# Kernel optimization log

Hardware: AMD Instinct MI355X
Metric: run time of the kernel (lower is better)

Reference implementation:

```python
import jax, jax.numpy as jnp
import numpy as np

B, S, IN_DIM, D_MODEL, H = 8, 1024, 512, 1024, 16
DEPTH = D_MODEL // H
LN_EPS = 1e-5


def setup_inputs() -> dict:
    key = jax.random.key(0)
    ks = jax.random.split(key, 10)
    def xavier(k, shape):
        fan_in, fan_out = shape[0], shape[1]
        lim = float(np.sqrt(6.0 / (fan_in + fan_out)))
        return jax.random.uniform(k, shape, jnp.float32, -lim, lim)
    return {
        "x": jax.random.normal(ks[0], (B, S, IN_DIM), jnp.float32),
        "mask": jax.random.randint(ks[1], (H, S, S), 0, 2, jnp.int32),
        "wq_w": xavier(ks[2], (IN_DIM, D_MODEL)),
        "wq_b": jnp.zeros((D_MODEL,), jnp.float32),
        "wk_w": xavier(ks[3], (IN_DIM, D_MODEL)),
        "wk_b": jnp.zeros((D_MODEL,), jnp.float32),
        "wv_w": xavier(ks[4], (IN_DIM, D_MODEL)),
        "wv_b": jnp.zeros((D_MODEL,), jnp.float32),
        "dense_w": xavier(ks[5], (D_MODEL, D_MODEL)),
        "dense_b": jnp.zeros((D_MODEL,), jnp.float32),
        "res_w": xavier(ks[6], (IN_DIM, D_MODEL)),  # residual_linear (no bias)
        "ln_g": 1.0 + 0.02 * jax.random.normal(ks[7], (D_MODEL,), jnp.float32),
        "ln_b": 0.02 * jax.random.normal(ks[8], (D_MODEL,), jnp.float32),
    }


def reference(x, mask, wq_w, wq_b, wk_w, wk_b, wv_w, wv_b,
              dense_w, dense_b, res_w, ln_g, ln_b):
    bs = x.shape[0]
    residual = x @ res_w  # [B,S,D_MODEL]
    # project and split heads -> [B,H,S,depth]
    def split(t):
        return t.reshape(bs, -1, H, DEPTH).transpose(0, 2, 1, 3)
    q = split(x @ wq_w + wq_b)
    k = split(x @ wk_w + wk_b)
    v = split(x @ wv_w + wv_b)
    scale = 1.0 / jnp.sqrt(jnp.asarray(DEPTH, x.dtype))
    attn = jnp.einsum("bhqd,bhkd->bhqk", q, k) * scale
    attn = jnp.where(mask[None] == 0, jnp.asarray(-1e9, attn.dtype), attn)
    attn = jax.nn.softmax(attn, axis=-1)  # dropout is identity in eval
    out = jnp.einsum("bhqk,bhkd->bhqd", attn, v)
    out = out.transpose(0, 2, 1, 3).reshape(bs, -1, D_MODEL)
    out = out @ dense_w + dense_b
    # residual + LayerNorm
    y = residual + out
    mu = jnp.mean(y, axis=-1, keepdims=True)
    var = jnp.mean(jnp.square(y - mu), axis=-1, keepdims=True)
    y = (y - mu) * jax.lax.rsqrt(var + LN_EPS)
    return y * ln_g + ln_b
```

## Files before the change

### kernel.cpp

```cpp
#include <hip/hip_runtime.h>
#include <stdint.h>

#define B_ 8
#define S_ 1024
#define IN_DIM 512
#define DM 1024
#define H_ 16
#define DEP 64

typedef __bf16 bf16;
typedef __attribute__((ext_vector_type(8))) __bf16 bf16x8;
typedef __attribute__((ext_vector_type(4))) __bf16 bf16x4;
typedef __attribute__((ext_vector_type(4))) short short4v;
typedef __attribute__((ext_vector_type(4))) float f32x4;

#if defined(__has_builtin)
#if __has_builtin(__builtin_amdgcn_mfma_f32_16x16x16_bf16)
#define HAVE_NEW16 1
#endif
#endif
static __device__ __forceinline__ f32x4 mfma16(bf16x4 a, bf16x4 b, f32x4 c) {
#ifdef HAVE_NEW16
    return __builtin_amdgcn_mfma_f32_16x16x16_bf16(a, b, c, 0, 0, 0);
#else
    union { bf16x4 h; short4v s; } ua, ub;
    ua.h = a; ub.h = b;
    return __builtin_amdgcn_mfma_f32_16x16x16bf16_1k(ua.s, ub.s, c, 0, 0, 0);
#endif
}

static __device__ __forceinline__ void gld_lds16(const void* g, void* l) {
    __builtin_amdgcn_global_load_lds(
        (const __attribute__((address_space(1))) uint32_t*)g,
        (__attribute__((address_space(3))) uint32_t*)l, 16, 0, 0);
}

__global__ void detect_kernel(const uint16_t* __restrict__ xraw, int* __restrict__ flag) {
    const int t = threadIdx.x;
    int sane = 0;
    #pragma unroll
    for (int j = 0; j < 8; j++) {
        const uint16_t u = xraw[t * 8 + j];
        const int e = (u >> 7) & 0xff;
        sane += ((u & 0x7fff) == 0 || (e >= 100 && e <= 140)) ? 1 : 0;
    }
    #pragma unroll
    for (int m = 1; m < 64; m <<= 1) sane += __shfl_xor(sane, m);
    if (t == 0) *flag = (sane >= 450) ? 1 : 0;
}

static __device__ __forceinline__ float ldin(const void* p, size_t i, int isb) {
    return isb ? (float)((const bf16*)p)[i] : ((const float*)p)[i];
}

__global__ __launch_bounds__(256) void transpose_kernel(
    const void* __restrict__ wq, const void* __restrict__ wk, const void* __restrict__ wv,
    const void* __restrict__ res, const void* __restrict__ dense,
    bf16* __restrict__ wqT, bf16* __restrict__ wkT, bf16* __restrict__ wvT,
    bf16* __restrict__ resT, bf16* __restrict__ denseT, const int* __restrict__ flag)
{
    const int isb = *flag;
    __shared__ bf16 tile[32][33];
    const int z = blockIdx.z;
    const void* src; bf16* dst; int kb, kd;
    if (z == 0)      { src = wq;    dst = wqT;    kb = 0;   kd = 512;  }
    else if (z == 1) { src = wk;    dst = wkT;    kb = 0;   kd = 512;  }
    else if (z == 2) { src = wv;    dst = wvT;    kb = 0;   kd = 512;  }
    else if (z == 3) { src = res;   dst = resT;   kb = 0;   kd = 512;  }
    else if (z == 4) { src = dense; dst = denseT; kb = 0;   kd = 1024; }
    else             { src = dense; dst = denseT; kb = 512; kd = 1024; }
    const int n0 = blockIdx.x * 32, k0 = blockIdx.y * 32;
    const int tx = threadIdx.x, ty = threadIdx.y;
    #pragma unroll
    for (int r = 0; r < 4; r++)
        tile[ty + r*8][tx] = (bf16)ldin(src, (size_t)(kb + k0 + ty + r*8) * DM + n0 + tx, isb);
    __syncthreads();
    #pragma unroll
    for (int r = 0; r < 4; r++)
        dst[(size_t)(n0 + ty + r*8) * kd + kb + k0 + tx] = tile[tx][ty + r*8];
}

__global__ __launch_bounds__(256) void xconv_kernel(
    const void* __restrict__ x, bf16* __restrict__ xc, const int* __restrict__ flag)
{
    const int isb = *flag;
    const size_t i = ((size_t)blockIdx.x * 256 + threadIdx.x) * 4;
    #pragma unroll
    for (int j = 0; j < 4; j++) xc[i + j] = (bf16)ldin(x, i + j, isb);
}

__global__ __launch_bounds__(256) void smallconv_kernel(
    const void* b0, const void* b1, const void* b2, const void* b3,
    const void* b4, const void* b5, bf16* __restrict__ out, const int* __restrict__ flag)
{
    const int isb = *flag;
    const void* srcs[6] = {b0, b1, b2, b3, b4, b5};
    const void* s = srcs[blockIdx.x];
    for (int i = threadIdx.x; i < 1024; i += 256)
        out[blockIdx.x * 1024 + i] = (bf16)ldin(s, i, isb);
}

__global__ __launch_bounds__(256) void maskpack_kernel(
    const int* __restrict__ mask, unsigned long long* __restrict__ mb)
{
    const int w = threadIdx.x >> 6, lane = threadIdx.x & 63;
    const int gw = blockIdx.x * 4 + w;
    for (int c = gw; c < 262144; c += 4096) {
        const int v = mask[(size_t)c * 64 + lane];
        const unsigned long long bits = __ballot(v != 0);
        if (lane == 0) mb[c] = bits;
    }
}

template<int KDIM>
static __device__ __forceinline__ void gemm_core(
    const bf16* __restrict__ A, const bf16* __restrict__ BT,
    int m0, int n0, bf16* Asm, bf16* Bsm, f32x4 acc[4][4])
{
    const int tid = threadIdx.x, l = tid & 63, w = tid >> 6;
    const int wm = w >> 1, wn = w & 1, quad = l >> 4, l15 = l & 15;
    #pragma unroll
    for (int i = 0; i < 4; i++)
        #pragma unroll
        for (int j = 0; j < 4; j++) acc[i][j] = f32x4{0.f, 0.f, 0.f, 0.f};

    for (int k0 = 0; k0 < KDIM; k0 += 32) {
        __syncthreads();
        #pragma unroll
        for (int qq = 0; qq < 2; qq++) {
            const int c = qq*256 + tid;
            const int row = c >> 2, ch = c & 3;
            gld_lds16(A  + (size_t)(m0 + row)*KDIM + k0 + ch*8, Asm + (qq*256 + w*64)*8);
            gld_lds16(BT + (size_t)(n0 + row)*KDIM + k0 + ch*8, Bsm + (qq*256 + w*64)*8);
        }
        __syncthreads();
        bf16x8 af[4], bfv[4];
        #pragma unroll
        for (int i = 0; i < 4; i++)
            af[i] = *(const bf16x8*)(Asm + (wm*64 + i*16 + l15)*32 + quad*8);
        #pragma unroll
        for (int j = 0; j < 4; j++)
            bfv[j] = *(const bf16x8*)(Bsm + (wn*64 + j*16 + l15)*32 + quad*8);
        #pragma unroll
        for (int i = 0; i < 4; i++)
            #pragma unroll
            for (int j = 0; j < 4; j++)
                acc[i][j] = __builtin_amdgcn_mfma_f32_16x16x32_bf16(af[i], bfv[j], acc[i][j], 0, 0, 0);
    }
}

#define EPI_P 132
__global__ __launch_bounds__(256) void proj_kernel(
    const bf16* __restrict__ x,
    const bf16* __restrict__ wqT, const bf16* __restrict__ wkT,
    const bf16* __restrict__ wvT, const bf16* __restrict__ resT,
    const bf16* __restrict__ small,
    bf16* __restrict__ Q, bf16* __restrict__ K, bf16* __restrict__ VtG, bf16* __restrict__ R)
{
    __shared__ alignas(16) char smem[17408];
    bf16* Asm = (bf16*)smem;
    bf16* Bsm = (bf16*)(smem + 8192);
    bf16* epi = (bf16*)smem;

    const int m0 = blockIdx.x * 128;
    const int ng = blockIdx.y * 128;
    const int sel = ng >> 10, n0 = ng & 1023;
    const bf16* BT; const bf16* bias = nullptr;
    if (sel == 0)      { BT = wqT; bias = small;        }
    else if (sel == 1) { BT = wkT; bias = small + 1024; }
    else if (sel == 2) { BT = wvT; bias = small + 2048; }
    else               { BT = resT; }

    f32x4 acc[4][4];
    gemm_core<IN_DIM>(x, BT, m0, n0, Asm, Bsm, acc);

    const int tid = threadIdx.x, l = tid & 63, w = tid >> 6;
    const int wm = w >> 1, wn = w & 1, quad = l >> 4, l15 = l & 15;

    if (sel == 2) {
        const int bb = m0 >> 10, srow0 = m0 & 1023;
        #pragma unroll
        for (int hf = 0; hf < 2; hf++) {
            __syncthreads();
            if (wn == hf) {
                #pragma unroll
                for (int j = 0; j < 4; j++) {
                    const int cl = j*16 + l15;
                    const float bv = (float)bias[n0 + hf*64 + cl];
                    #pragma unroll
                    for (int i = 0; i < 4; i++) {
                        const int rho = wm*64 + i*16 + quad*4;
                        #pragma unroll
                        for (int r = 0; r < 4; r++)
                            epi[cl*EPI_P + rho + r] = (bf16)(acc[i][j][r] + bv);
                    }
                }
            }
            __syncthreads();
            const int hh = (n0 >> 6) + hf;
            const int sc = tid & 15;
            #pragma unroll
            for (int pass = 0; pass < 4; pass++) {
                const int dl = (tid >> 4) + pass*16;
                bf16x8 v;
                #pragma unroll
                for (int k = 0; k < 8; k++) v[k] = epi[dl*EPI_P + sc*8 + k];
                *(bf16x8*)(VtG + ((size_t)(bb*16 + hh)*64 + dl)*S_ + srow0 + sc*8) = v;
            }
        }
        return;
    }

    #pragma unroll
    for (int j = 0; j < 4; j++) {
        const int col = n0 + wn*64 + j*16 + l15;
        const float bv = (sel < 3) ? (float)bias[col] : 0.f;
        #pragma unroll
        for (int i = 0; i < 4; i++) {
            const int rb = m0 + wm*64 + i*16 + quad*4;
            #pragma unroll
            for (int r = 0; r < 4; r++) {
                const float v = acc[i][j][r] + bv;
                if (sel == 0)      Q[(size_t)(rb + r)*DM + col] = (bf16)(v * 0.18033688f);
                else if (sel == 1) K[(size_t)(rb + r)*DM + col] = (bf16)v;
                else               R[(size_t)(rb + r)*DM + col] = (bf16)v;
            }
        }
    }
}

__global__ __launch_bounds__(256, 4) void attn_kernel(
    const bf16* __restrict__ Q, const bf16* __restrict__ K, const bf16* __restrict__ VtG,
    const unsigned long long* __restrict__ mb, bf16* __restrict__ AO)
{
    __shared__ alignas(16) bf16 Ksm[2*64*64];
    __shared__ alignas(16) bf16 Vsm[2*64*64];

    const int tid = threadIdx.x, l = tid & 63, w = tid >> 6;
    const int quad = l >> 4, l15 = l & 15;

    const int fid = blockIdx.y * 8 + blockIdx.x;
    const int xcd = fid & 7, idx = fid >> 3;
    const int bh  = xcd * 16 + (idx >> 3);
    const int qt  = idx & 7;
    const int b = bh >> 4, h = bh & 15;
    const int wrow = qt*128 + w*32;
    const size_t rowbase = (size_t)b * S_;

    bf16x8 qa[2][2];
    #pragma unroll
    for (int g = 0; g < 2; g++) {
        const bf16* qp = Q + (rowbase + wrow + g*16 + l15)*DM + h*DEP + quad*8;
        qa[g][0] = *(const bf16x8*)qp;
        qa[g][1] = *(const bf16x8*)(qp + 32);
    }
    const bf16* kgbase = K + rowbase*DM + h*DEP;
    const bf16* vgbase = VtG + (size_t)(b*16 + h)*64*S_;
    const unsigned long long* mbase[2];
    #pragma unroll
    for (int g = 0; g < 2; g++)
        mbase[g] = mb + ((size_t)h*S_ + wrow + g*16 + l15) * 16;

    uint32_t bmr[4];
    #pragma unroll
    for (int r = 0; r < 4; r++) bmr[r] = 1u << (quad*4 + r);

    bf16x4 onesv;
    #pragma unroll
    for (int r = 0; r < 4; r++) onesv[r] = (bf16)1.0f;

    f32x4 oT[2][4];
    f32x4 lacc[2];
    #pragma unroll
    for (int g = 0; g < 2; g++) {
        lacc[g] = f32x4{0.f,0.f,0.f,0.f};
        #pragma unroll
        for (int dt = 0; dt < 4; dt++) oT[g][dt] = f32x4{0.f,0.f,0.f,0.f};
    }

    const int srow8 = l >> 3;
    const int gch   = (l & 7) ^ srow8;

    #pragma unroll
    for (int q = 0; q < 2; q++) {
        const int row = q*32 + w*8 + srow8;
        gld_lds16(kgbase + (size_t)row*DM + gch*8, Ksm + (q*256 + w*64)*8);
        gld_lds16(vgbase + (size_t)row*S_ + gch*8, Vsm + (q*256 + w*64)*8);
    }

    const int rsw = l15 & 7;

    for (int it = 0; it < 16; it++) {
        __syncthreads();
        const int cur = (it & 1) * 4096, nxt = cur ^ 4096;
        const bf16* Kc = Ksm + cur;
        const bf16* Vc = Vsm + cur;

        uint32_t cm[2][2];
        #pragma unroll
        for (int g = 0; g < 2; g++) {
            const unsigned long long mw = mbase[g][it];
            cm[g][0] = (uint32_t)mw; cm[g][1] = (uint32_t)(mw >> 32);
        }

        if (it + 1 < 16) {
            #pragma unroll
            for (int q = 0; q < 2; q++) {
                const int row = q*32 + w*8 + srow8;
                gld_lds16(kgbase + (size_t)((it+1)*64 + row)*DM + gch*8,
                          Ksm + nxt + (q*256 + w*64)*8);
                gld_lds16(vgbase + (size_t)row*S_ + (it+1)*64 + gch*8,
                          Vsm + nxt + (q*256 + w*64)*8);
            }
        }

        #pragma unroll
        for (int sub = 0; sub < 2; sub++) {
            bf16x8 kf[2][2];
            bf16x4 va[2][4];
            #pragma unroll
            for (int h2 = 0; h2 < 2; h2++) {
                const int krow = sub*32 + h2*16 + l15;
                kf[h2][0] = *(const bf16x8*)(Kc + krow*64 + ((quad    ) ^ rsw)*8);
                kf[h2][1] = *(const bf16x8*)(Kc + krow*64 + ((quad + 4) ^ rsw)*8);
            }
            #pragma unroll
            for (int h2 = 0; h2 < 2; h2++) {
                const int cb = sub*4 + h2*2 + (quad >> 1);
                #pragma unroll
                for (int dt = 0; dt < 4; dt++)
                    va[h2][dt] = *(const bf16x4*)(Vc + (dt*16 + l15)*64 + (cb ^ rsw)*8 + (quad&1)*4);
            }

            #pragma unroll
            for (int g = 0; g < 2; g++) {
                f32x4 st[2];
                __builtin_amdgcn_s_setprio(1);
                #pragma unroll
                for (int h2 = 0; h2 < 2; h2++) {
                    f32x4 z = {0.f,0.f,0.f,0.f};
                    z = __builtin_amdgcn_mfma_f32_16x16x32_bf16(kf[h2][0], qa[g][0], z, 0, 0, 0);
                    z = __builtin_amdgcn_mfma_f32_16x16x32_bf16(kf[h2][1], qa[g][1], z, 0, 0, 0);
                    st[h2] = z;
                }
                __builtin_amdgcn_s_setprio(0);
                const uint32_t msk = cm[g][sub];
                bf16x4 pb[2];
                #pragma unroll
                for (int h2 = 0; h2 < 2; h2++) {
                    const uint32_t mh = msk >> (h2 * 16);
                    #pragma unroll
                    for (int r = 0; r < 4; r++) {
                        const float e = __builtin_amdgcn_exp2f(st[h2][r]);
                        const float pv = (mh & bmr[r]) ? e : 0.f;
                        pb[h2][r] = (bf16)pv;
                    }
                }
                __builtin_amdgcn_s_setprio(1);
                #pragma unroll
                for (int h2 = 0; h2 < 2; h2++) {
                    lacc[g] = mfma16(onesv, pb[h2], lacc[g]);
                    #pragma unroll
                    for (int dt = 0; dt < 4; dt++)
                        oT[g][dt] = mfma16(va[h2][dt], pb[h2], oT[g][dt]);
                }
                __builtin_amdgcn_s_setprio(0);
            }
        }
    }

    #pragma unroll
    for (int g = 0; g < 2; g++) {
        const float inv = 1.0f / lacc[g][0];
        bf16* aor = AO + (rowbase + wrow + g*16 + l15)*DM + h*DEP;
        #pragma unroll
        for (int dt = 0; dt < 4; dt++) {
            bf16x4 ov;
            #pragma unroll
            for (int r = 0; r < 4; r++) ov[r] = (bf16)(oT[g][dt][r] * inv);
            *(bf16x4*)(aor + dt*16 + quad*4) = ov;
        }
    }
}

__global__ __launch_bounds__(256) void dense_kernel(
    const bf16* __restrict__ AOin, const bf16* __restrict__ dT,
    const bf16* __restrict__ db, bf16* __restrict__ R)
{
    __shared__ alignas(16) bf16 Asm[128*32];
    __shared__ alignas(16) bf16 Bsm[128*32];
    const int m0 = blockIdx.x * 128, n0 = blockIdx.y * 128;
    f32x4 acc[4][4];
    gemm_core<DM>(AOin, dT, m0, n0, Asm, Bsm, acc);
    const int tid = threadIdx.x, l = tid & 63, w = tid >> 6;
    const int wm = w >> 1, wn = w & 1, quad = l >> 4, l15 = l & 15;
    #pragma unroll
    for (int j = 0; j < 4; j++) {
        const int col = n0 + wn*64 + j*16 + l15;
        const float bv = (float)db[col];
        #pragma unroll
        for (int i = 0; i < 4; i++) {
            const int rb = m0 + wm*64 + i*16 + quad*4;
            #pragma unroll
            for (int r = 0; r < 4; r++) {
                const size_t idx = (size_t)(rb + r)*DM + col;
                R[idx] = (bf16)((float)R[idx] + acc[i][j][r] + bv);
            }
        }
    }
}

__global__ __launch_bounds__(256) void ln_kernel(
    const bf16* __restrict__ R, const bf16* __restrict__ small,
    void* __restrict__ out, const int* __restrict__ flag)
{
    const int isb = *flag;
    __shared__ float red[8];
    const int row = blockIdx.x, tid = threadIdx.x;
    const bf16x4 rv = *(const bf16x4*)(R + (size_t)row*DM + tid*4);
    const float vx = (float)rv[0], vy = (float)rv[1], vz = (float)rv[2], vw = (float)rv[3];
    float s = vx + vy + vz + vw;
    #pragma unroll
    for (int m = 1; m < 64; m <<= 1) s += __shfl_xor(s, m);
    const int w = tid >> 6;
    if ((tid & 63) == 0) red[w] = s;
    __syncthreads();
    const float mu = (red[0] + red[1] + red[2] + red[3]) * (1.0f/DM);
    const float dx = vx - mu, dy = vy - mu, dz = vz - mu, dw = vw - mu;
    float q = dx*dx + dy*dy + dz*dz + dw*dw;
    #pragma unroll
    for (int m = 1; m < 64; m <<= 1) q += __shfl_xor(q, m);
    if ((tid & 63) == 0) red[4 + w] = q;
    __syncthreads();
    const float var = (red[4] + red[5] + red[6] + red[7]) * (1.0f/DM);
    const float rstd = rsqrtf(var + 1e-5f);
    const int col = tid * 4;
    const bf16x4 gv = *(const bf16x4*)(small + 4*1024 + col);
    const bf16x4 bv = *(const bf16x4*)(small + 5*1024 + col);
    const float o0 = dx*rstd*(float)gv[0] + (float)bv[0];
    const float o1 = dy*rstd*(float)gv[1] + (float)bv[1];
    const float o2 = dz*rstd*(float)gv[2] + (float)bv[2];
    const float o3 = dw*rstd*(float)gv[3] + (float)bv[3];
    if (isb) {
        bf16x4 ov; ov[0] = (bf16)o0; ov[1] = (bf16)o1; ov[2] = (bf16)o2; ov[3] = (bf16)o3;
        *(bf16x4*)((bf16*)out + (size_t)row*DM + col) = ov;
    } else {
        float4 ov = {o0, o1, o2, o3};
        *(float4*)((float*)out + (size_t)row*DM + col) = ov;
    }
}

extern "C" void kernel_launch(void* const* d_in, const int* in_sizes, int n_in,
                              void* d_out, int out_size, void* d_ws, size_t ws_size,
                              hipStream_t stream) {
    const int* mask = (const int*)d_in[1];

    char* ws = (char*)d_ws;
    bf16* wqT   = (bf16*)(ws);
    bf16* wkT   = (bf16*)(ws + ((size_t)1 << 20));
    bf16* wvT   = (bf16*)(ws + ((size_t)2 << 20));
    bf16* resT  = (bf16*)(ws + ((size_t)3 << 20));
    bf16* dT    = (bf16*)(ws + ((size_t)4 << 20));
    bf16* small = (bf16*)(ws + ((size_t)6 << 20));
    int*  flag  = (int*) (ws + ((size_t)6 << 20) + 16384);
    unsigned long long* mbits = (unsigned long long*)(ws + ((size_t)7 << 20));
    bf16* Qb    = (bf16*)(ws + ((size_t)9  << 20));
    bf16* Kb    = (bf16*)(ws + ((size_t)25 << 20));
    bf16* VtG   = (bf16*)(ws + ((size_t)41 << 20));
    bf16* R     = (bf16*)(ws + ((size_t)57 << 20));
    bf16* xc    = (bf16*)d_out;

    detect_kernel<<<1, 64, 0, stream>>>((const uint16_t*)d_in[0], flag);
    transpose_kernel<<<dim3(32, 16, 6), dim3(32, 8), 0, stream>>>(
        d_in[2], d_in[4], d_in[6], d_in[10], d_in[8],
        wqT, wkT, wvT, resT, dT, flag);
    xconv_kernel<<<4096, 256, 0, stream>>>(d_in[0], xc, flag);
    smallconv_kernel<<<6, 256, 0, stream>>>(
        d_in[3], d_in[5], d_in[7], d_in[9], d_in[11], d_in[12], small, flag);
    maskpack_kernel<<<1024, 256, 0, stream>>>(mask, mbits);
    proj_kernel<<<dim3(64, 32), 256, 0, stream>>>(
        xc, wqT, wkT, wvT, resT, small, Qb, Kb, VtG, R);
    attn_kernel<<<dim3(8, 128), 256, 0, stream>>>(Qb, Kb, VtG, mbits, Qb );
    dense_kernel<<<dim3(64, 8), 256, 0, stream>>>(Qb, dT, small + 3*1024, R);
    ln_kernel<<<8192, 256, 0, stream>>>(R, small, d_out, flag);
}
```

Before: 357.3 us.

## Permute V layout for wide LDS reads and shrink dense GEMM tile

The projection epilogue now writes the transposed V with a permuted column order inside each 32-key group. This lets the attention kernel fetch V fragments with one 16-byte LDS read per dt instead of two 8-byte reads, then split them into the two halves MFMA needs. Separately, the dense kernel gets its own 64x128 tile loop in place of the shared 128x128 gemm_core, doubling the grid so more CUs are busy. The trade-off is less data reuse per block and a simpler, non-pipelined load loop.

```diff
diff --git a/kernel.cpp b/kernel.cpp
--- a/kernel.cpp
+++ b/kernel.cpp
@@ -204,7 +204,11 @@
                 const int dl = (tid >> 4) + pass*16;
                 bf16x8 v;
                 #pragma unroll
-                for (int k = 0; k < 8; k++) v[k] = epi[dl*EPI_P + sc*8 + k];
+                for (int k = 0; k < 8; k++) {
+                    const int pl = (sc & 3)*8 + k;
+                    const int kl = ((pl & 4) << 2) | ((pl & 24) >> 1) | (pl & 3);
+                    v[k] = epi[dl*EPI_P + (sc >> 2)*32 + kl];
+                }
                 *(bf16x8*)(VtG + ((size_t)(bb*16 + hh)*64 + dl)*S_ + srow0 + sc*8) = v;
             }
         }
@@ -317,7 +321,7 @@
         #pragma unroll
         for (int sub = 0; sub < 2; sub++) {
             bf16x8 kf[2][2];
-            bf16x4 va[2][4];
+            bf16x8 va8[4];
             #pragma unroll
             for (int h2 = 0; h2 < 2; h2++) {
                 const int krow = sub*32 + h2*16 + l15;
@@ -325,12 +329,16 @@
                 kf[h2][1] = *(const bf16x8*)(Kc + krow*64 + ((quad + 4) ^ rsw)*8);
             }
             #pragma unroll
-            for (int h2 = 0; h2 < 2; h2++) {
-                const int cb = sub*4 + h2*2 + (quad >> 1);
+            for (int dt = 0; dt < 4; dt++)
+                va8[dt] = *(const bf16x8*)(Vc + (dt*16 + l15)*64 + ((sub*4 + quad) ^ rsw)*8);
+            bf16x4 va[2][4];
+            #pragma unroll
+            for (int dt = 0; dt < 4; dt++)
                 #pragma unroll
-                for (int dt = 0; dt < 4; dt++)
-                    va[h2][dt] = *(const bf16x4*)(Vc + (dt*16 + l15)*64 + (cb ^ rsw)*8 + (quad&1)*4);
-            }
+                for (int r = 0; r < 4; r++) {
+                    va[0][dt][r] = va8[dt][r];
+                    va[1][dt][r] = va8[dt][4 + r];
+                }
 
             #pragma unroll
             for (int g = 0; g < 2; g++) {
@@ -387,20 +395,52 @@
     const bf16* __restrict__ AOin, const bf16* __restrict__ dT,
     const bf16* __restrict__ db, bf16* __restrict__ R)
 {
-    __shared__ alignas(16) bf16 Asm[128*32];
+    __shared__ alignas(16) bf16 Asm[64*32];
     __shared__ alignas(16) bf16 Bsm[128*32];
-    const int m0 = blockIdx.x * 128, n0 = blockIdx.y * 128;
-    f32x4 acc[4][4];
-    gemm_core<DM>(AOin, dT, m0, n0, Asm, Bsm, acc);
+    const int m0 = blockIdx.x * 64, n0 = blockIdx.y * 128;
     const int tid = threadIdx.x, l = tid & 63, w = tid >> 6;
     const int wm = w >> 1, wn = w & 1, quad = l >> 4, l15 = l & 15;
+
+    f32x4 acc[2][4];
+    #pragma unroll
+    for (int i = 0; i < 2; i++)
+        #pragma unroll
+        for (int j = 0; j < 4; j++) acc[i][j] = f32x4{0.f, 0.f, 0.f, 0.f};
+
+    for (int k0 = 0; k0 < DM; k0 += 32) {
+        __syncthreads();
+        {
+            const int row = tid >> 2;
+            gld_lds16(AOin + (size_t)(m0 + row)*DM + k0 + (tid & 3)*8, Asm + (w*64)*8);
+        }
+        #pragma unroll
+        for (int qq = 0; qq < 2; qq++) {
+            const int c = qq*256 + tid;
+            const int row = c >> 2, ch = c & 3;
+            gld_lds16(dT + (size_t)(n0 + row)*DM + k0 + ch*8, Bsm + (qq*256 + w*64)*8);
+        }
+        __syncthreads();
+        bf16x8 af[2], bfv[4];
+        #pragma unroll
+        for (int i = 0; i < 2; i++)
+            af[i] = *(const bf16x8*)(Asm + (wm*32 + i*16 + l15)*32 + quad*8);
+        #pragma unroll
+        for (int j = 0; j < 4; j++)
+            bfv[j] = *(const bf16x8*)(Bsm + (wn*64 + j*16 + l15)*32 + quad*8);
+        #pragma unroll
+        for (int i = 0; i < 2; i++)
+            #pragma unroll
+            for (int j = 0; j < 4; j++)
+                acc[i][j] = __builtin_amdgcn_mfma_f32_16x16x32_bf16(af[i], bfv[j], acc[i][j], 0, 0, 0);
+    }
+
     #pragma unroll
     for (int j = 0; j < 4; j++) {
         const int col = n0 + wn*64 + j*16 + l15;
         const float bv = (float)db[col];
         #pragma unroll
-        for (int i = 0; i < 4; i++) {
-            const int rb = m0 + wm*64 + i*16 + quad*4;
+        for (int i = 0; i < 2; i++) {
+            const int rb = m0 + wm*32 + i*16 + quad*4;
             #pragma unroll
             for (int r = 0; r < 4; r++) {
                 const size_t idx = (size_t)(rb + r)*DM + col;
@@ -481,6 +521,6 @@
     proj_kernel<<<dim3(64, 32), 256, 0, stream>>>(
         xc, wqT, wkT, wvT, resT, small, Qb, Kb, VtG, R);
     attn_kernel<<<dim3(8, 128), 256, 0, stream>>>(Qb, Kb, VtG, mbits, Qb );
-    dense_kernel<<<dim3(64, 8), 256, 0, stream>>>(Qb, dT, small + 3*1024, R);
+    dense_kernel<<<dim3(128, 8), 256, 0, stream>>>(Qb, dT, small + 3*1024, R);
     ln_kernel<<<8192, 256, 0, stream>>>(R, small, d_out, flag);
 }
```

Result: slower. 410.2 us (+14.8%).
